# Kernel optimization log

Hardware: AMD Instinct MI355X
Metric: run time of the kernel (lower is better)

The kernel has to match this reference:

```python
import jax, jax.numpy as jnp
import numpy as np

NEG = -1e30  # log(0) surrogate that stays finite in fp32
BLANK = 0


def setup_inputs() -> dict:
    key = jax.random.key(0)
    k1, k2 = jax.random.split(key)
    B, T, V, L = 32, 1024, 1024, 256
    logits = jax.random.normal(k1, (B, T, V), dtype=jnp.float32)
    log_probs = jax.nn.log_softmax(logits, axis=-1)  # module expects log-probs
    labels = jax.random.randint(k2, (B, L), 1, V, dtype=jnp.int32)  # avoid blank=0
    input_lens = jnp.full((B,), T, dtype=jnp.int32)
    label_lens = jnp.full((B,), L, dtype=jnp.int32)
    return {"log_probs": log_probs, "labels": labels,
            "input_lens": input_lens, "label_lens": label_lens}


def _ctc_loss_sum(log_probs, labels, input_lens, label_lens, blank=BLANK):
    """CTC forward DP (alpha recursion) in log space; reduction='sum', zero_infinity=True."""
    B, T, V = log_probs.shape
    L = labels.shape[1]
    S = 2 * L + 1  # extended label: blank l1 blank l2 ... blank

    ext = jnp.full((B, S), blank, dtype=labels.dtype)
    ext = ext.at[:, 1::2].set(labels)
    # skip transition s-2 -> s allowed iff ext[s] != blank and ext[s] != ext[s-2]
    skip = jnp.concatenate(
        [jnp.zeros((B, 2), dtype=bool),
         (ext[:, 2:] != blank) & (ext[:, 2:] != ext[:, :-2])], axis=1)

    lp_tbv = jnp.transpose(log_probs, (1, 0, 2))  # 'btv->tbv' as in the module

    emit0 = jnp.take_along_axis(lp_tbv[0], ext, axis=1)  # [B,S]
    alpha0 = jnp.full((B, S), NEG, dtype=log_probs.dtype)
    alpha0 = alpha0.at[:, 0].set(emit0[:, 0]).at[:, 1].set(emit0[:, 1])

    neg1 = jnp.full((B, 1), NEG, dtype=log_probs.dtype)
    neg2 = jnp.full((B, 2), NEG, dtype=log_probs.dtype)

    def step(alpha, inputs):
        lp_t, t = inputs  # lp_t: [B,V]
        em = jnp.take_along_axis(lp_t, ext, axis=1)  # [B,S]
        a1 = alpha
        a2 = jnp.concatenate([neg1, alpha[:, :-1]], axis=1)
        a3 = jnp.where(skip, jnp.concatenate([neg2, alpha[:, :-2]], axis=1), NEG)
        new = jnp.logaddexp(jnp.logaddexp(a1, a2), a3) + em
        # freeze alpha once past this sample's input length
        new = jnp.where((t < input_lens)[:, None], new, alpha)
        return new, None

    ts = jnp.arange(1, T)
    alpha, _ = jax.lax.scan(step, alpha0, (lp_tbv[1:], ts))

    s_last = 2 * label_lens  # final blank state index per sample
    a_last = jnp.take_along_axis(alpha, s_last[:, None], axis=1)[:, 0]
    a_prev = jnp.take_along_axis(alpha, (s_last - 1)[:, None], axis=1)[:, 0]
    loss_b = -jnp.logaddexp(a_last, a_prev)
    loss_b = jnp.where(loss_b > 1e29, 0.0, loss_b)  # zero_infinity=True
    return jnp.sum(loss_b)


def reference(log_probs, labels, input_lens, label_lens):
    return _ctc_loss_sum(log_probs, labels, input_lens, label_lens)
```

## Files before the change

kernel.cpp:

```cpp
#include <hip/hip_runtime.h>


constexpr int B_ = 32, T_ = 1024, V_ = 1024, L_ = 256;
constexpr int S_ = 2 * L_ + 1;
constexpr int CH = 16;
constexpr int NCHUNK = 64;
constexpr int NBUF = 4;
constexpr float LN2F = 0.6931471805599453f;

typedef const __attribute__((address_space(1))) unsigned int* gp_t;
typedef __attribute__((address_space(3))) unsigned int* lp_t;

__global__ __launch_bounds__(256, 4) void ctc_gather(
    float* __restrict__ lp, const int* __restrict__ labels,
    float* __restrict__ blanks)
{
    const int wave = threadIdx.x >> 6;
    const int lane = threadIdx.x & 63;
    const int r = blockIdx.x * 4 + wave;
    const int b = r >> 10;
    float* row = lp + (size_t)r * V_;
    const int* labb = labels + b * L_;

    const int4 e = *(const int4*)(labb + 4 * lane);
    const float v0 = row[e.x];
    const float v1 = row[e.y];
    const float v2 = row[e.z];
    const float v3 = row[e.w];
    const float vb = row[0];
    float4 q;
    q.x = __expf(v0); q.y = __expf(v1); q.z = __expf(v2); q.w = __expf(v3);
    const float qb = __expf(vb);
    __syncthreads();
    *(float4*)(row + 4 * lane) = q;
    if (lane == 0) {
        const int t = r & (T_ - 1);
        blanks[(r & ~(T_ - 1)) + ((t + T_ - 1) & (T_ - 1))] = qb;
    }
}

__global__ __launch_bounds__(128) void ctc_dp(
    const float* __restrict__ Q, const float* __restrict__ blanks,
    const int* __restrict__ labels, const int* __restrict__ input_lens,
    const int* __restrict__ label_lens, float* __restrict__ out)
{
    __shared__ float blk[T_];
    __shared__ float buf[NBUF][CH][256];
    __shared__ int Pf, Cf;
    const int b    = blockIdx.x;
    const int tid  = threadIdx.x;
    const int lane = tid & 63;
    const int wv   = tid >> 6;
    const float* Qb  = Q + (size_t)b * T_ * V_;
    const float* blg = blanks + b * T_;
    const int*  labb = labels + b * L_;
    const int il = input_lens[b];
    const int ll = label_lens[b];
    const int tend = il < T_ ? il : T_;

    if (tid == 0) { Pf = 0; Cf = 0; }
    __syncthreads();

    if (wv == 1) {
        #pragma unroll
        for (int i = 0; i < 4; ++i)
            __builtin_amdgcn_global_load_lds((gp_t)(blg + 256 * i + 4 * lane),
                                             (lp_t)&blk[256 * i], 16, 0, 0);
        #pragma unroll
        for (int i = 0; i < CH; ++i) {
            int t = 1 + i; if (t > T_ - 1) t = T_ - 1;
            __builtin_amdgcn_global_load_lds(
                (gp_t)(Qb + (size_t)t * V_ + 4 * lane),
                (lp_t)&buf[0][i][0], 16, 0, 0);
        }
        for (int c = 0; c < NCHUNK; ++c) {
            if (c + 1 < NCHUNK) {
                while (__hip_atomic_load(&Cf, __ATOMIC_ACQUIRE,
                                         __HIP_MEMORY_SCOPE_WORKGROUP) < c + 2 - NBUF) {}
                const int cb = (c + 1) & (NBUF - 1);
                #pragma unroll
                for (int i = 0; i < CH; ++i) {
                    int t = 1 + (c + 1) * CH + i; if (t > T_ - 1) t = T_ - 1;
                    __builtin_amdgcn_global_load_lds(
                        (gp_t)(Qb + (size_t)t * V_ + 4 * lane),
                        (lp_t)&buf[cb][i][0], 16, 0, 0);
                }
                asm volatile("s_waitcnt vmcnt(16)" ::: "memory");
            } else {
                asm volatile("s_waitcnt vmcnt(0)" ::: "memory");
            }
            if (lane == 0)
                __hip_atomic_store(&Pf, c + 1, __ATOMIC_RELEASE,
                                   __HIP_MEMORY_SCOPE_WORKGROUP);
        }
    } else {
        const int4 e  = *(const int4*)(labb + 4 * lane);
        const int  ep = (lane > 0) ? labb[4 * lane - 1] : -1;
        const float kf0 = ((8 * lane + 1) >= 3 && e.x != ep) ? 1.f : 0.f;
        const float kf1 = (e.y != e.x) ? 1.f : 0.f;
        const float kf2 = (e.z != e.y) ? 1.f : 0.f;
        const float kf3 = (e.w != e.z) ? 1.f : 0.f;
        const float bl0 = blg[T_ - 1];
        const float q00 = Qb[0];
        float p0 = (lane == 0) ? bl0 : 0.f;
        float p1 = (lane == 0) ? q00 : 0.f;
        float p2 = 0.f, p3 = 0.f, p4 = 0.f, p5 = 0.f,
              p6 = 0.f, p7 = 0.f, p8 = 0.f;
        int Esc = 0;
        float pm1 = 0.f;

        auto rescale = [&]() {
            float m = fmaxf(fmaxf(fmaxf(fmaxf(p0, p1), fmaxf(p2, p3)),
                                  fmaxf(fmaxf(p4, p5), fmaxf(p6, p7))), p8);
            #pragma unroll
            for (int off = 32; off >= 1; off >>= 1)
                m = fmaxf(m, __shfl_xor(m, off));
            const unsigned eb = (__float_as_uint(m) >> 23) & 0xffu;
            if (eb >= 1u && eb <= 253u) {
                const float sf = __uint_as_float((254u - eb) << 23);
                p0 *= sf; p1 *= sf; p2 *= sf; p3 *= sf; p4 *= sf;
                p5 *= sf; p6 *= sf; p7 *= sf; p8 *= sf; pm1 *= sf;
                Esc += 127 - (int)eb;
            }
        };

        for (int c = 0; c < NCHUNK; ++c) {
            while (__hip_atomic_load(&Pf, __ATOMIC_ACQUIRE,
                                     __HIP_MEMORY_SCOPE_WORKGROUP) <= c) {}
            const float* bufc = &buf[c & (NBUF - 1)][0][0];
            float4 bv;
            #pragma unroll
            for (int i = 0; i < CH; ++i) {
                if ((i & 3) == 0) bv = *(const float4*)&blk[c * CH + i];
                const float qb = ((i & 3) == 0) ? bv.x : ((i & 3) == 1) ? bv.y
                               : ((i & 3) == 2) ? bv.z : bv.w;
                const int t = 1 + c * CH + i;
                if (t < tend) {
                    const float4 q = *(const float4*)(bufc + i * 256 + 4 * lane);
                    const float n0 = (p0 + pm1) * qb;
                    const float n1 = fmaf(kf0, pm1, p1 + p0) * q.x;
                    const float n2 = (p2 + p1) * qb;
                    const float n3 = fmaf(kf1, p1, p3 + p2) * q.y;
                    const float n4 = (p4 + p3) * qb;
                    const float n5 = fmaf(kf2, p3, p5 + p4) * q.z;
                    const float n6 = (p6 + p5) * qb;
                    const float n7 = fmaf(kf3, p5, p7 + p6) * q.w;
                    const float n8 = (p8 + p7) * qb;
                    p0 = n0; p1 = n1; p2 = n2; p3 = n3; p4 = n4;
                    p5 = n5; p6 = n6; p7 = n7; p8 = n8;
                    pm1 = __shfl_up(p7, 1);
                    if (lane == 0) pm1 = 0.f;
                }
                if (i == 7) rescale();
            }
            rescale();
            if (lane == 0)
                __hip_atomic_store(&Cf, c + 1, __ATOMIC_RELEASE,
                                   __HIP_MEMORY_SCOPE_WORKGROUP);
        }

        const int sl = 2 * ll;
        auto pick = [&](int s) -> float {
            if (s == 512) return __shfl(p8, 63);
            const int r = s & 7;
            float v = p0;
            v = (r == 1) ? p1 : v; v = (r == 2) ? p2 : v;
            v = (r == 3) ? p3 : v; v = (r == 4) ? p4 : v;
            v = (r == 5) ? p5 : v; v = (r == 6) ? p6 : v;
            v = (r == 7) ? p7 : v;
            return __shfl(v, s >> 3);
        };
        const float la = pick(sl);
        const float lb = pick(sl - 1);
        if (lane == 0) {
            const float tot = la + lb;
            float loss = (float)Esc * LN2F - __logf(tot);
            if (!(loss <= 1e29f)) loss = 0.f;
            atomicAdd(out, loss);
        }
    }
}

extern "C" void kernel_launch(void* const* d_in, const int* in_sizes, int n_in,
                              void* d_out, int out_size, void* d_ws, size_t ws_size,
                              hipStream_t stream) {
    float*       lp     = (float*)d_in[0];
    const int*   labels = (const int*)d_in[1];
    const int*   il     = (const int*)d_in[2];
    const int*   ll     = (const int*)d_in[3];
    float* out    = (float*)d_out;
    float* blanks = (float*)d_ws;

    hipMemsetAsync(out, 0, sizeof(float), stream);
    ctc_gather<<<dim3(B_ * T_ / 4), dim3(256), 0, stream>>>(lp, labels, blanks);
    ctc_dp<<<dim3(B_), dim3(128), 0, stream>>>(lp, blanks, labels, il, ll, out);
}
```

Measured before the change: 342.5 us.

## Defer rescale factors into emissions and pipeline LDS loads and lane shuffle

The DP loop no longer multiplies all nine state registers during each rescale. It computes the scale factor a few steps early (snap) and folds it into the emission probabilities at the next half-chunk boundary, which takes the cross-lane max reduction off the critical dependency chain. It also double-buffers the per-step LDS float4 loads and computes n7 first, so the cross-lane shuffle for the next step overlaps with the remaining arithmetic. The scale exponent is now biased toward larger values (318-eb clamp), which relies on values staying in range for the few unscaled steps and adds some numeric risk.

```diff
diff --git a/kernel.cpp b/kernel.cpp
--- a/kernel.cpp
+++ b/kernel.cpp
@@ -108,35 +108,48 @@
               p6 = 0.f, p7 = 0.f, p8 = 0.f;
         int Esc = 0;
         float pm1 = 0.f;
-
-        auto rescale = [&]() {
+        float sfP = 1.f, sfM = 1.f;
+
+        auto snap = [&]() -> float {
             float m = fmaxf(fmaxf(fmaxf(fmaxf(p0, p1), fmaxf(p2, p3)),
                                   fmaxf(fmaxf(p4, p5), fmaxf(p6, p7))), p8);
             #pragma unroll
             for (int off = 32; off >= 1; off >>= 1)
                 m = fmaxf(m, __shfl_xor(m, off));
             const unsigned eb = (__float_as_uint(m) >> 23) & 0xffu;
-            if (eb >= 1u && eb <= 253u) {
-                const float sf = __uint_as_float((254u - eb) << 23);
-                p0 *= sf; p1 *= sf; p2 *= sf; p3 *= sf; p4 *= sf;
-                p5 *= sf; p6 *= sf; p7 *= sf; p8 *= sf; pm1 *= sf;
-                Esc += 127 - (int)eb;
+            if (eb >= 1u && eb <= 254u) {
+                unsigned k = 318u - eb;
+                if (k > 254u) k = 254u;
+                Esc += (int)k - 127;
+                return __uint_as_float(k << 23);
             }
+            return 1.f;
         };
 
         for (int c = 0; c < NCHUNK; ++c) {
             while (__hip_atomic_load(&Pf, __ATOMIC_ACQUIRE,
                                      __HIP_MEMORY_SCOPE_WORKGROUP) <= c) {}
-            const float* bufc = &buf[c & (NBUF - 1)][0][0];
+            const float* base = &buf[c & (NBUF - 1)][0][0] + 4 * lane;
+            float4 qp0 = *(const float4*)(base);
+            float4 qp1 = *(const float4*)(base + 256);
             float4 bv;
             #pragma unroll
             for (int i = 0; i < CH; ++i) {
                 if ((i & 3) == 0) bv = *(const float4*)&blk[c * CH + i];
-                const float qb = ((i & 3) == 0) ? bv.x : ((i & 3) == 1) ? bv.y
-                               : ((i & 3) == 2) ? bv.z : bv.w;
+                float qb = ((i & 3) == 0) ? bv.x : ((i & 3) == 1) ? bv.y
+                         : ((i & 3) == 2) ? bv.z : bv.w;
+                float4 q = qp0;
+                qp0 = qp1;
+                if (i < CH - 2)
+                    qp1 = *(const float4*)(base + (i + 2) * 256);
+                if (i == 0) { q.x *= sfP; q.y *= sfP; q.z *= sfP; q.w *= sfP; qb *= sfP; }
+                if (i == 8) { q.x *= sfM; q.y *= sfM; q.z *= sfM; q.w *= sfM; qb *= sfM; }
                 const int t = 1 + c * CH + i;
                 if (t < tend) {
-                    const float4 q = *(const float4*)(bufc + i * 256 + 4 * lane);
+                    const float n7 = fmaf(kf3, p5, p7 + p6) * q.w;
+                    const float n8 = (p8 + p7) * qb;
+                    float pm1n = __shfl_up(n7, 1);
+                    if (lane == 0) pm1n = 0.f;
                     const float n0 = (p0 + pm1) * qb;
                     const float n1 = fmaf(kf0, pm1, p1 + p0) * q.x;
                     const float n2 = (p2 + p1) * qb;
@@ -144,20 +157,18 @@
                     const float n4 = (p4 + p3) * qb;
                     const float n5 = fmaf(kf2, p3, p5 + p4) * q.z;
                     const float n6 = (p6 + p5) * qb;
-                    const float n7 = fmaf(kf3, p5, p7 + p6) * q.w;
-                    const float n8 = (p8 + p7) * qb;
                     p0 = n0; p1 = n1; p2 = n2; p3 = n3; p4 = n4;
-                    p5 = n5; p6 = n6; p7 = n7; p8 = n8;
-                    pm1 = __shfl_up(p7, 1);
-                    if (lane == 0) pm1 = 0.f;
+                    p5 = n5; p6 = n6; p7 = n7; p8 = n8; pm1 = pm1n;
                 }
-                if (i == 7) rescale();
+                if (i == 4)  sfM = snap();
+                if (i == 12) sfP = snap();
             }
-            rescale();
             if (lane == 0)
                 __hip_atomic_store(&Cf, c + 1, __ATOMIC_RELEASE,
                                    __HIP_MEMORY_SCOPE_WORKGROUP);
         }
+        p0 *= sfP; p1 *= sfP; p2 *= sfP; p3 *= sfP; p4 *= sfP;
+        p5 *= sfP; p6 *= sfP; p7 *= sfP; p8 *= sfP;
 
         const int sl = 2 * ll;
         auto pick = [&](int s) -> float {
```

Result: no change. 336.2 us (-1.9%).
